# Kernel tuning notes

Measured on AMD Instinct MI355X. Metric: run time of the kernel, lower is better.

The kernel has to match this reference:

```python
import jax, jax.numpy as jnp
import numpy as np

B, L, D_MODEL = 4, 2048, 1024
N_HEADS, FEAT, HEAD_DIM = 16, 16, 64
CHUNK = 128
EPS = 1e-12


def taylor_exp(x):
    """2nd-order Taylor feature map of exp(q.k/sqrt(d)).
    x: (b, h, l, f) -> (b, h, l, 1 + f + f*f)"""
    f = x.shape[-1]
    r2 = jnp.sqrt(jnp.asarray(2.0, x.dtype))
    rd = jnp.sqrt(jnp.asarray(float(f), x.dtype))      # sqrt(d)
    rrd = jnp.sqrt(rd)                                  # d**0.25
    x2 = (x[..., :, None] * x[..., None, :]).reshape(*x.shape[:-1], f * f) / r2
    ones = jnp.ones_like(x[..., :1])
    return jnp.concatenate([ones, x / rrd, x2 / rd], axis=-1)


def setup_inputs() -> dict:
    key = jax.random.key(0)
    k1, k2, k3, k4, k5 = jax.random.split(key, 5)
    s = 0.02
    return {
        "hidden_states": jax.random.normal(k1, (B, L, D_MODEL), jnp.float32),
        "Wq": jax.random.normal(k2, (N_HEADS * FEAT, D_MODEL), jnp.float32) * s,
        "Wk": jax.random.normal(k3, (N_HEADS * FEAT, D_MODEL), jnp.float32) * s,
        "Wv": jax.random.normal(k4, (N_HEADS * HEAD_DIM, D_MODEL), jnp.float32) * s,
        "Wo": jax.random.normal(k5, (D_MODEL, N_HEADS * HEAD_DIM), jnp.float32) * s,
    }


def reference(hidden_states, Wq, Wk, Wv, Wo):
    b, l, _ = hidden_states.shape
    # projections (Linear without bias: x @ W.T)
    q = (hidden_states @ Wq.T).reshape(b, l, N_HEADS, FEAT).transpose(0, 2, 1, 3)
    k = (hidden_states @ Wk.T).reshape(b, l, N_HEADS, FEAT).transpose(0, 2, 1, 3)
    v = (hidden_states @ Wv.T).reshape(b, l, N_HEADS, HEAD_DIM).transpose(0, 2, 1, 3)

    qf = taylor_exp(q)  # (b, h, l, De) with De = 1 + f + f^2 = 273
    kf = taylor_exp(k)
    De = qf.shape[-1]

    # chunked causal linear attention: same math as cumulative kv-state
    n = l // CHUNK
    qc = jnp.moveaxis(qf.reshape(b, N_HEADS, n, CHUNK, De), 2, 0)       # (n,b,h,c,De)
    kc = jnp.moveaxis(kf.reshape(b, N_HEADS, n, CHUNK, De), 2, 0)
    vc = jnp.moveaxis(v.reshape(b, N_HEADS, n, CHUNK, HEAD_DIM), 2, 0)
    mask = jnp.tril(jnp.ones((CHUNK, CHUNK), qf.dtype))

    def step(carry, xs):
        S, z = carry                       # S: (b,h,De,e), z: (b,h,De)
        qi, ki, vi = xs
        attn = jnp.einsum('bhid,bhjd->bhij', qi, ki) * mask
        num = jnp.einsum('bhij,bhje->bhie', attn, vi) \
            + jnp.einsum('bhid,bhde->bhie', qi, S)
        den = attn.sum(-1) + jnp.einsum('bhid,bhd->bhi', qi, z)
        yi = num / (den[..., None] + EPS)
        S = S + jnp.einsum('bhjd,bhje->bhde', ki, vi)
        z = z + ki.sum(2)
        return (S, z), yi

    S0 = jnp.zeros((b, N_HEADS, De, HEAD_DIM), qf.dtype)
    z0 = jnp.zeros((b, N_HEADS, De), qf.dtype)
    _, ys = jax.lax.scan(step, (S0, z0), (qc, kc, vc))
    y = jnp.moveaxis(ys, 0, 2).reshape(b, N_HEADS, l, HEAD_DIM)          # (b,h,l,e)
    y = y.transpose(0, 2, 1, 3).reshape(b, l, N_HEADS * HEAD_DIM)        # (b,l,h*e)
    return y @ Wo.T
```

## Files before the change

### kernel.cpp

```cpp
#include <hip/hip_runtime.h>
#include <hip/hip_bf16.h>

#define BB 4
#define LL 2048
#define DM 1024
#define NH 16
#define FEAT 16
#define HD 64
#define CHUNK 128
#define NCHUNK 16
#define NEXT 65
#define SROW 18720
#define EPS 1e-12f
#define INV_R2RD 0.17677669529663688f
#define QKVLD 1536

typedef short bf16x8_t __attribute__((ext_vector_type(8)));
typedef float f32x4_t  __attribute__((ext_vector_type(4)));

__device__ __forceinline__ float b2f(unsigned short u) {
    union { unsigned int i; float f; } x; x.i = ((unsigned int)u) << 16; return x.f;
}
__device__ __forceinline__ unsigned short f2b(float f) {
    __hip_bfloat16 h = __float2bfloat16(f);
    return *reinterpret_cast<unsigned short*>(&h);
}

__global__ __launch_bounds__(256)
void cast_all(const float* __restrict__ hs, const float* __restrict__ wq,
              const float* __restrict__ wk, const float* __restrict__ wv,
              const float* __restrict__ wo, unsigned short* __restrict__ hs_bf,
              unsigned short* __restrict__ wqkv, unsigned short* __restrict__ wo_bf)
{
    const int i = (blockIdx.x * 256 + threadIdx.x) * 4;
    const float* s; unsigned short* d;
    if (i < 8388608)       { s = hs + i;             d = hs_bf + i; }
    else if (i < 8650752)  { s = wq + (i - 8388608); d = wqkv + (i - 8388608); }
    else if (i < 8912896)  { s = wk + (i - 8650752); d = wqkv + 262144 + (i - 8650752); }
    else if (i < 9961472)  { s = wv + (i - 8912896); d = wqkv + 524288 + (i - 8912896); }
    else if (i < 11010048) { s = wo + (i - 9961472); d = wo_bf + (i - 9961472); }
    else return;
    float4 v = *(const float4*)s;
    ushort4 o; o.x = f2b(v.x); o.y = f2b(v.y); o.z = f2b(v.z); o.w = f2b(v.w);
    *(ushort4*)d = o;
}

template <typename OutT>
__global__ __launch_bounds__(512, 2)
void gemm_bf16_8ph(const unsigned short* __restrict__ A, const unsigned short* __restrict__ Bw,
                   OutT* __restrict__ C, int K, int lda, int ldb, int ldc)
{
    __shared__ unsigned short lds[65536];
    const int tid  = threadIdx.x;
    const int wid  = tid >> 6, lane = tid & 63;
    const int wm   = wid >> 2, wn = wid & 3;
    const int ml   = lane & 15, quad = lane >> 4;
    const int nwg = gridDim.x * gridDim.y;
    const int lin = blockIdx.y * gridDim.x + blockIdx.x;
    const int swz_id = (lin & 7) * (nwg >> 3) + (lin >> 3);
    const int m0   = (swz_id / gridDim.x) * 256, n0 = (swz_id % gridDim.x) * 256;
    const int NT   = K >> 6;

    const int srow  = tid >> 3;
    const int scol  = ((tid & 7) ^ (srow & 7)) << 3;
    const int wbase = wid << 9;

    auto stage_half = [&](int t, int isB, int h) {
        const unsigned short* g0 = isB ? Bw : A;
        const int ld = isB ? ldb : lda;
        const int rb = (isB ? n0 : m0) + h * 128 + srow;
        const int k0 = t << 6;
        unsigned short* lb = lds + (isB ? 32768 : 0) + ((t & 1) << 14) + (h << 13) + wbase;
#pragma unroll
        for (int l = 0; l < 2; ++l) {
            const unsigned short* g = g0 + (size_t)(rb + l * 64) * ld + k0 + scol;
            __builtin_amdgcn_global_load_lds((const __attribute__((address_space(1))) void*)g,
                                             (__attribute__((address_space(3))) void*)(lb + l * 4096),
                                             16, 0, 0);
        }
    };

    f32x4_t acc[8][4];
#pragma unroll
    for (int i = 0; i < 8; ++i)
#pragma unroll
        for (int j = 0; j < 4; ++j) acc[i][j] = (f32x4_t){0.f, 0.f, 0.f, 0.f};

    stage_half(0, 0, 0); stage_half(0, 1, 0); stage_half(0, 0, 1); stage_half(0, 1, 1);
    stage_half(1, 0, 0); stage_half(1, 1, 0); stage_half(1, 0, 1);
    asm volatile("s_waitcnt vmcnt(6)" ::: "memory");
    __builtin_amdgcn_s_barrier();

    const int swz  = (ml & 7) << 3;
    const int c0   = (quad << 3) ^ swz;
    const int c1   = (32 + (quad << 3)) ^ swz;
    const int arow = ml << 6;

    bf16x8_t aA[4][2], bLo[2][2], bHi[2][2];

    for (int t = 0; t < NT; ++t) {
        const int ab = (t & 1) << 14;
        const int bb = 32768 + ((t & 1) << 14);

#pragma unroll
        for (int m = 0; m < 4; ++m) {
            const int r = ab + ((2 * m + wm) << 10) + arow;
            aA[m][0] = *(const bf16x8_t*)&lds[r + c0];
            aA[m][1] = *(const bf16x8_t*)&lds[r + c1];
        }
#pragma unroll
        for (int n = 0; n < 2; ++n) {
            const int r = bb + ((4 * n + wn) << 10) + arow;
            bLo[n][0] = *(const bf16x8_t*)&lds[r + c0];
            bLo[n][1] = *(const bf16x8_t*)&lds[r + c1];
        }
        if (t + 1 < NT) stage_half(t + 1, 1, 1);
        __builtin_amdgcn_s_barrier();
        asm volatile("s_waitcnt lgkmcnt(0)" ::: "memory");
        __builtin_amdgcn_sched_barrier(0);
        __builtin_amdgcn_s_setprio(1);
#pragma unroll
        for (int m = 0; m < 4; ++m)
#pragma unroll
            for (int n = 0; n < 2; ++n) {
                acc[m][n] = __builtin_amdgcn_mfma_f32_16x16x32_bf16(aA[m][0], bLo[n][0], acc[m][n], 0, 0, 0);
                acc[m][n] = __builtin_amdgcn_mfma_f32_16x16x32_bf16(aA[m][1], bLo[n][1], acc[m][n], 0, 0, 0);
            }
        __builtin_amdgcn_s_setprio(0);
        __builtin_amdgcn_s_barrier();

#pragma unroll
        for (int n = 0; n < 2; ++n) {
            const int r = bb + ((4 * (n + 2) + wn) << 10) + arow;
            bHi[n][0] = *(const bf16x8_t*)&lds[r + c0];
            bHi[n][1] = *(const bf16x8_t*)&lds[r + c1];
        }
        if (t + 2 < NT) stage_half(t + 2, 0, 0);
        __builtin_amdgcn_s_barrier();
        asm volatile("s_waitcnt lgkmcnt(0)" ::: "memory");
        __builtin_amdgcn_sched_barrier(0);
        __builtin_amdgcn_s_setprio(1);
#pragma unroll
        for (int m = 0; m < 4; ++m)
#pragma unroll
            for (int n = 0; n < 2; ++n) {
                acc[m][2 + n] = __builtin_amdgcn_mfma_f32_16x16x32_bf16(aA[m][0], bHi[n][0], acc[m][2 + n], 0, 0, 0);
                acc[m][2 + n] = __builtin_amdgcn_mfma_f32_16x16x32_bf16(aA[m][1], bHi[n][1], acc[m][2 + n], 0, 0, 0);
            }
        __builtin_amdgcn_s_setprio(0);
        __builtin_amdgcn_s_barrier();

#pragma unroll
        for (int m = 0; m < 4; ++m) {
            const int r = ab + ((2 * (m + 4) + wm) << 10) + arow;
            aA[m][0] = *(const bf16x8_t*)&lds[r + c0];
            aA[m][1] = *(const bf16x8_t*)&lds[r + c1];
        }
        if (t + 2 < NT) stage_half(t + 2, 1, 0);
        __builtin_amdgcn_s_barrier();
        asm volatile("s_waitcnt lgkmcnt(0)" ::: "memory");
        __builtin_amdgcn_sched_barrier(0);
        __builtin_amdgcn_s_setprio(1);
#pragma unroll
        for (int m = 0; m < 4; ++m)
#pragma unroll
            for (int n = 0; n < 2; ++n) {
                acc[4 + m][2 + n] = __builtin_amdgcn_mfma_f32_16x16x32_bf16(aA[m][0], bHi[n][0], acc[4 + m][2 + n], 0, 0, 0);
                acc[4 + m][2 + n] = __builtin_amdgcn_mfma_f32_16x16x32_bf16(aA[m][1], bHi[n][1], acc[4 + m][2 + n], 0, 0, 0);
            }
        __builtin_amdgcn_s_setprio(0);
        __builtin_amdgcn_s_barrier();

        if (t + 2 < NT) stage_half(t + 2, 0, 1);
        __builtin_amdgcn_s_barrier();
        asm volatile("s_waitcnt lgkmcnt(0)" ::: "memory");
        __builtin_amdgcn_sched_barrier(0);
        __builtin_amdgcn_s_setprio(1);
#pragma unroll
        for (int m = 0; m < 4; ++m)
#pragma unroll
            for (int n = 0; n < 2; ++n) {
                acc[4 + m][n] = __builtin_amdgcn_mfma_f32_16x16x32_bf16(aA[m][0], bLo[n][0], acc[4 + m][n], 0, 0, 0);
                acc[4 + m][n] = __builtin_amdgcn_mfma_f32_16x16x32_bf16(aA[m][1], bLo[n][1], acc[4 + m][n], 0, 0, 0);
            }
        __builtin_amdgcn_s_setprio(0);
        if (t + 2 < NT)      asm volatile("s_waitcnt vmcnt(6)" ::: "memory");
        else if (t + 1 < NT) asm volatile("s_waitcnt vmcnt(0)" ::: "memory");
        __builtin_amdgcn_s_barrier();
    }

#pragma unroll
    for (int m = 0; m < 8; ++m) {
        const int rbase = m0 + (2 * m + wm) * 16 + quad * 4;
#pragma unroll
        for (int n = 0; n < 4; ++n) {
            const int col = n0 + (4 * n + wn) * 16 + ml;
#pragma unroll
            for (int r = 0; r < 4; ++r) {
                const float v = acc[m][n][r];
                if constexpr (sizeof(OutT) == 2) {
                    ((unsigned short*)C)[(size_t)(rbase + r) * ldc + col] = f2b(v);
                } else {
                    ((float*)C)[(size_t)(rbase + r) * ldc + col] = v;
                }
            }
        }
    }
}

__global__ __launch_bounds__(512, 2)
void gemm_bf16_128x256(const unsigned short* __restrict__ A, const unsigned short* __restrict__ Bw,
                       float* __restrict__ C, int K, int lda, int ldb, int ldc)
{
    __shared__ unsigned short lds[49152];
    const int tid  = threadIdx.x;
    const int wid  = tid >> 6, lane = tid & 63;
    const int wm   = wid >> 2, wn = wid & 3;
    const int ml   = lane & 15, quad = lane >> 4;
    const int nwg = gridDim.x * gridDim.y;
    const int lin = blockIdx.y * gridDim.x + blockIdx.x;
    const int swz_id = (lin & 7) * (nwg >> 3) + (lin >> 3);
    const int m0   = (swz_id / gridDim.x) * 128, n0 = (swz_id % gridDim.x) * 256;
    const int NT   = K >> 6;

    const int srow  = tid >> 3;
    const int scol  = ((tid & 7) ^ (srow & 7)) << 3;
    const int wbase = wid << 9;

    auto stage_unit = [&](int t, int isB, int u) {
        const unsigned short* g0 = isB ? Bw : A;
        const int ld = isB ? ldb : lda;
        const int rb = (isB ? n0 : m0) + u * 64 + srow;
        const int k0 = t << 6;
        unsigned short* lb = lds + (isB ? 16384 : 0) + ((t & 1) << (isB ? 14 : 13))
                             + (u << 12) + wbase;
        const unsigned short* g = g0 + (size_t)rb * ld + k0 + scol;
        __builtin_amdgcn_global_load_lds((const __attribute__((address_space(1))) void*)g,
                                         (__attribute__((address_space(3))) void*)lb, 16, 0, 0);
    };

    f32x4_t acc[4][4];
#pragma unroll
    for (int i = 0; i < 4; ++i)
#pragma unroll
        for (int j = 0; j < 4; ++j) acc[i][j] = (f32x4_t){0.f, 0.f, 0.f, 0.f};

    stage_unit(0, 0, 0); stage_unit(0, 0, 1);
    stage_unit(0, 1, 0); stage_unit(0, 1, 1); stage_unit(0, 1, 2); stage_unit(0, 1, 3);
    stage_unit(1, 0, 0); stage_unit(1, 0, 1);
    stage_unit(1, 1, 0); stage_unit(1, 1, 1);
    asm volatile("s_waitcnt vmcnt(4)" ::: "memory");
    __builtin_amdgcn_s_barrier();

    const int swz  = (ml & 7) << 3;
    const int c0   = (quad << 3) ^ swz;
    const int c1   = (32 + (quad << 3)) ^ swz;
    const int arow = ml << 6;

    bf16x8_t aA[4][2], bF[2][2];

    for (int t = 0; t < NT; ++t) {
        const int ab = (t & 1) << 13;
        const int bb = 16384 + ((t & 1) << 14);

#pragma unroll
        for (int m = 0; m < 4; ++m) {
            const int r = ab + ((2 * m + wm) << 10) + arow;
            aA[m][0] = *(const bf16x8_t*)&lds[r + c0];
            aA[m][1] = *(const bf16x8_t*)&lds[r + c1];
        }
#pragma unroll
        for (int n = 0; n < 2; ++n) {
            const int r = bb + ((4 * n + wn) << 10) + arow;
            bF[n][0] = *(const bf16x8_t*)&lds[r + c0];
            bF[n][1] = *(const bf16x8_t*)&lds[r + c1];
        }
        if (t + 1 < NT) { stage_unit(t + 1, 1, 2); stage_unit(t + 1, 1, 3); }
        __builtin_amdgcn_s_barrier();
        asm volatile("s_waitcnt lgkmcnt(0)" ::: "memory");
        __builtin_amdgcn_sched_barrier(0);
        __builtin_amdgcn_s_setprio(1);
#pragma unroll
        for (int m = 0; m < 4; ++m)
#pragma unroll
            for (int n = 0; n < 2; ++n) {
                acc[m][n] = __builtin_amdgcn_mfma_f32_16x16x32_bf16(aA[m][0], bF[n][0], acc[m][n], 0, 0, 0);
                acc[m][n] = __builtin_amdgcn_mfma_f32_16x16x32_bf16(aA[m][1], bF[n][1], acc[m][n], 0, 0, 0);
            }
        __builtin_amdgcn_s_setprio(0);
        __builtin_amdgcn_s_barrier();

#pragma unroll
        for (int n = 0; n < 2; ++n) {
            const int r = bb + ((4 * (n + 2) + wn) << 10) + arow;
            bF[n][0] = *(const bf16x8_t*)&lds[r + c0];
            bF[n][1] = *(const bf16x8_t*)&lds[r + c1];
        }
        if (t + 2 < NT) {
            stage_unit(t + 2, 0, 0); stage_unit(t + 2, 0, 1);
            stage_unit(t + 2, 1, 0); stage_unit(t + 2, 1, 1);
        }
        __builtin_amdgcn_s_barrier();
        asm volatile("s_waitcnt lgkmcnt(0)" ::: "memory");
        __builtin_amdgcn_sched_barrier(0);
        __builtin_amdgcn_s_setprio(1);
#pragma unroll
        for (int m = 0; m < 4; ++m)
#pragma unroll
            for (int n = 0; n < 2; ++n) {
                acc[m][2 + n] = __builtin_amdgcn_mfma_f32_16x16x32_bf16(aA[m][0], bF[n][0], acc[m][2 + n], 0, 0, 0);
                acc[m][2 + n] = __builtin_amdgcn_mfma_f32_16x16x32_bf16(aA[m][1], bF[n][1], acc[m][2 + n], 0, 0, 0);
            }
        __builtin_amdgcn_s_setprio(0);
        if (t + 2 < NT)      asm volatile("s_waitcnt vmcnt(4)" ::: "memory");
        else if (t + 1 < NT) asm volatile("s_waitcnt vmcnt(0)" ::: "memory");
        __builtin_amdgcn_s_barrier();
    }

#pragma unroll
    for (int m = 0; m < 4; ++m) {
        const int rbase = m0 + (2 * m + wm) * 16 + quad * 4;
#pragma unroll
        for (int n = 0; n < 4; ++n) {
            const int col = n0 + (4 * n + wn) * 16 + ml;
#pragma unroll
            for (int r = 0; r < 4; ++r)
                C[(size_t)(rbase + r) * ldc + col] = acc[m][n][r];
        }
    }
}

__global__ __launch_bounds__(256)
void state_kernel(const unsigned short* __restrict__ qkv, unsigned short* __restrict__ STg)
{
    __shared__ unsigned short KT[16 * 136];
    __shared__ unsigned short VT[80 * 136];

    const int x = blockIdx.x;
    const int c = x & 15, bh = x >> 4;
    const int b = bh >> 4, h = bh & 15;
    const int tid = threadIdx.x;
    const int wave = tid >> 6, lane = tid & 63;
    const int ml = lane & 15, kg8 = (lane >> 4) * 8;
    const int quad4 = (lane >> 4) * 4;
    const size_t rowbase = (size_t)(b * LL + c * CHUNK);
    const size_t Sbase = (size_t)x * SROW;

    {
        const int row = tid >> 1, half = tid & 1;
        uint4 kv = *(const uint4*)(qkv + (rowbase + row) * QKVLD + 256 + h * 16 + half * 8);
        const unsigned short* kp = (const unsigned short*)&kv;
#pragma unroll
        for (int i = 0; i < 8; ++i) KT[(half * 8 + i) * 136 + row] = kp[i];
#pragma unroll
        for (int cc = 0; cc < 4; ++cc) {
            uint4 vv = *(const uint4*)(qkv + (rowbase + row) * QKVLD + 512 + h * 64 + half * 32 + cc * 8);
            const unsigned short* vp = (const unsigned short*)&vv;
#pragma unroll
            for (int i = 0; i < 8; ++i) VT[(half * 32 + cc * 8 + i) * 136 + row] = vp[i];
        }
        if (half == 0) {
            VT[64 * 136 + row] = 0x3F80;
        } else {
#pragma unroll
            for (int e = 65; e < 80; ++e) VT[e * 136 + row] = 0;
        }
    }
    __syncthreads();

    bf16x8_t bfr[5][4];
#pragma unroll
    for (int nt = 0; nt < 5; ++nt)
#pragma unroll
        for (int ks = 0; ks < 4; ++ks)
            bfr[nt][ks] = *(const bf16x8_t*)&VT[(nt * 16 + ml) * 136 + ks * 32 + kg8];

    for (int mt = wave; mt < 18; mt += 4) {
        const int d = mt * 16 + ml;
        bf16x8_t af[4];
#pragma unroll
        for (int ks = 0; ks < 4; ++ks) {
            const int jb = ks * 32 + kg8;
            unsigned short o[8];
            if (d >= 24 && d < 280) {
                const int e = d - 24, a = e >> 4, bq = e & 15;
                bf16x8_t ka = *(const bf16x8_t*)&KT[a  * 136 + jb];
                bf16x8_t kb = *(const bf16x8_t*)&KT[bq * 136 + jb];
#pragma unroll
                for (int j = 0; j < 8; ++j)
                    o[j] = f2b(b2f((unsigned short)ka[j]) * b2f((unsigned short)kb[j]) * INV_R2RD);
            } else if (d == 0) {
#pragma unroll
                for (int j = 0; j < 8; ++j) o[j] = 0x3F80;
            } else if (d <= 16) {
                bf16x8_t kx = *(const bf16x8_t*)&KT[(d - 1) * 136 + jb];
#pragma unroll
                for (int j = 0; j < 8; ++j) o[j] = f2b(b2f((unsigned short)kx[j]) * 0.5f);
            } else {
#pragma unroll
                for (int j = 0; j < 8; ++j) o[j] = 0;
            }
            af[ks] = *(const bf16x8_t*)o;
        }
        f32x4_t acc[5];
#pragma unroll
        for (int nt = 0; nt < 5; ++nt) acc[nt] = (f32x4_t){0.f, 0.f, 0.f, 0.f};
        __builtin_amdgcn_s_setprio(1);
#pragma unroll
        for (int nt = 0; nt < 5; ++nt)
#pragma unroll
            for (int ks = 0; ks < 4; ++ks)
                acc[nt] = __builtin_amdgcn_mfma_f32_16x16x32_bf16(af[ks], bfr[nt][ks], acc[nt], 0, 0, 0);
        __builtin_amdgcn_s_setprio(0);
#pragma unroll
        for (int nt = 0; nt < 5; ++nt) {
            ushort4 pk;
            pk.x = f2b(acc[nt][0]); pk.y = f2b(acc[nt][1]);
            pk.z = f2b(acc[nt][2]); pk.w = f2b(acc[nt][3]);
            if (nt < 4) {
                *(ushort4*)(STg + Sbase + (size_t)mt * 1040 + (nt * 16 + ml) * 16 + quad4) = pk;
            } else if (ml == 0) {
                *(ushort4*)(STg + Sbase + (size_t)mt * 1040 + 1024 + quad4) = pk;
            }
        }
    }
}

__global__ __launch_bounds__(256)
void scan_S(unsigned short* __restrict__ STg) {
    const int bh  = blockIdx.y;
    const int idx = blockIdx.x * 256 + threadIdx.x;
    if (idx >= SROW / 8) return;
    const size_t base = (size_t)bh * NCHUNK * SROW + (size_t)idx * 8;
    uint4 v[NCHUNK];
#pragma unroll
    for (int c = 0; c < NCHUNK; ++c)
        v[c] = *(const uint4*)(STg + base + (size_t)c * SROW);
    float acc[8] = {};
#pragma unroll
    for (int c = 0; c < NCHUNK; ++c) {
        const unsigned short* vp = (const unsigned short*)&v[c];
        uint4 o;
        unsigned short* op = (unsigned short*)&o;
#pragma unroll
        for (int i = 0; i < 8; ++i) { op[i] = f2b(acc[i]); acc[i] += b2f(vp[i]); }
        *(uint4*)(STg + base + (size_t)c * SROW) = o;
    }
}

#define OFF_VT 0
#define OFF_QP 0
#define OFF_KP 5120
#define OFF_A  10880

__global__ __launch_bounds__(256)
void out_kernel(const unsigned short* __restrict__ qkv_ro, const unsigned short* __restrict__ STg,
                unsigned short* __restrict__ qkv_w)
{
    __shared__ unsigned short smem[28288];

    const int x = blockIdx.x;
    const int c = x & 15, bh = x >> 4;
    const int b = bh >> 4, h = bh & 15;
    const int tid = threadIdx.x;
    const int w = tid >> 6, lane = tid & 63;
    const int ml = lane & 15, quad = lane >> 4, kg8 = quad * 8;
    const size_t rowbase = (size_t)(b * LL + c * CHUNK);
    const size_t Sbase = (size_t)x * SROW;

    const unsigned short* stp = STg + Sbase + (size_t)(quad >> 1) * 1040 + (quad & 1) * 8;
    bf16x8_t stf[3][5];
    auto ldst = [&](int kq, int slot) {
#pragma unroll
        for (int nt = 0; nt < 5; ++nt)
            stf[slot][nt] = *(const bf16x8_t*)(stp + (size_t)kq * 2080 + (nt * 16 + ml) * 16);
    };

    const int row = tid >> 1, half = tid & 1;
    uint4 qv = *(const uint4*)(qkv_ro + (rowbase + row) * QKVLD + h * 16 + half * 8);
    uint4 kv = *(const uint4*)(qkv_ro + (rowbase + row) * QKVLD + 256 + h * 16 + half * 8);
    uint4 vreg[4];
#pragma unroll
    for (int cc = 0; cc < 4; ++cc)
        vreg[cc] = *(const uint4*)(qkv_ro + (rowbase + row) * QKVLD + 512 + h * 64 + half * 32 + cc * 8);
    ldst(0, 0);
    ldst(1, 1);

    *(uint4*)&smem[OFF_QP + row * 40 + half * 8] = qv;
    *(uint4*)&smem[OFF_QP + row * 40 + 16 + half * 8] = (uint4){0, 0, 0, 0};
    *(uint4*)&smem[OFF_KP + row * 40 + half * 8] = kv;
    *(uint4*)&smem[OFF_KP + row * 40 + 16 + half * 8] = (uint4){0, 0, 0, 0};
    __syncthreads();

    {
        bf16x8_t q0 = *(const bf16x8_t*)&smem[OFF_QP + (w * 32 + ml) * 40 + kg8];
        bf16x8_t q1 = *(const bf16x8_t*)&smem[OFF_QP + (w * 32 + 16 + ml) * 40 + kg8];
#pragma unroll
        for (int nt = 0; nt < 8; ++nt) {
            bf16x8_t kf = *(const bf16x8_t*)&smem[OFF_KP + (nt * 16 + ml) * 40 + kg8];
            f32x4_t a0 = __builtin_amdgcn_mfma_f32_16x16x32_bf16(q0, kf, (f32x4_t){0,0,0,0}, 0, 0, 0);
            f32x4_t a1 = __builtin_amdgcn_mfma_f32_16x16x32_bf16(q1, kf, (f32x4_t){0,0,0,0}, 0, 0, 0);
            const int j = nt * 16 + ml;
#pragma unroll
            for (int r = 0; r < 4; ++r) {
                int i0 = w * 32 + quad * 4 + r;
                float s0 = a0[r] * 0.25f;
                float v0 = (j <= i0) ? (1.f + s0 + 0.5f * s0 * s0) : 0.f;
                smem[OFF_A + i0 * 136 + j] = f2b(v0);
                int i1 = i0 + 16;
                float s1 = a1[r] * 0.25f;
                float v1 = (j <= i1) ? (1.f + s1 + 0.5f * s1 * s1) : 0.f;
                smem[OFF_A + i1 * 136 + j] = f2b(v1);
            }
        }
    }
    const int r0 = w * 32 + ml, r1 = r0 + 16;
    float qA[16], qB[16];
    {
        bf16x8_t t0 = *(const bf16x8_t*)&smem[OFF_QP + r0 * 40];
        bf16x8_t t1 = *(const bf16x8_t*)&smem[OFF_QP + r0 * 40 + 8];
        bf16x8_t t2 = *(const bf16x8_t*)&smem[OFF_QP + r1 * 40];
        bf16x8_t t3 = *(const bf16x8_t*)&smem[OFF_QP + r1 * 40 + 8];
#pragma unroll
        for (int i = 0; i < 8; ++i) {
            qA[i] = b2f((unsigned short)t0[i]); qA[8 + i] = b2f((unsigned short)t1[i]);
            qB[i] = b2f((unsigned short)t2[i]); qB[8 + i] = b2f((unsigned short)t3[i]);
        }
    }
    float qselA[8], qselB[8];
#pragma unroll
    for (int j = 0; j < 8; ++j) {
        qselA[j] = (quad & 1) ? qA[j] : qA[8 + j];
        qselB[j] = (quad & 1) ? qB[j] : qB[8 + j];
    }
    __syncthreads();

    {
#pragma unroll
        for (int cc = 0; cc < 4; ++cc) {
            const unsigned short* vp = (const unsigned short*)&vreg[cc];
#pragma unroll
            for (int i = 0; i < 8; ++i) smem[OFF_VT + (half * 32 + cc * 8 + i) * 136 + row] = vp[i];
        }
        if (half == 0) {
            smem[OFF_VT + 64 * 136 + row] = 0x3F80;
        } else {
#pragma unroll
            for (int e = 65; e < 80; ++e) smem[OFF_VT + e * 136 + row] = 0;
        }
    }
    __syncthreads();

    f32x4_t acc[2][5];
#pragma unroll
    for (int mt = 0; mt < 2; ++mt)
#pragma unroll
        for (int nt = 0; nt < 5; ++nt) acc[mt][nt] = (f32x4_t){0.f, 0.f, 0.f, 0.f};

    ldst(2, 2);

#pragma unroll
    for (int ks = 0; ks < 4; ++ks) {
        bf16x8_t af0 = *(const bf16x8_t*)&smem[OFF_A + (w * 32 + ml) * 136 + ks * 32 + kg8];
        bf16x8_t af1 = *(const bf16x8_t*)&smem[OFF_A + (w * 32 + 16 + ml) * 136 + ks * 32 + kg8];
        __builtin_amdgcn_s_setprio(1);
#pragma unroll
        for (int nt = 0; nt < 5; ++nt) {
            bf16x8_t bv = *(const bf16x8_t*)&smem[OFF_VT + (nt * 16 + ml) * 136 + ks * 32 + kg8];
            acc[0][nt] = __builtin_amdgcn_mfma_f32_16x16x32_bf16(af0, bv, acc[0][nt], 0, 0, 0);
            acc[1][nt] = __builtin_amdgcn_mfma_f32_16x16x32_bf16(af1, bv, acc[1][nt], 0, 0, 0);
        }
        __builtin_amdgcn_s_setprio(0);
    }

#pragma unroll
    for (int kq = 0; kq < 9; ++kq) {
        bf16x8_t qf[2];
#pragma unroll
        for (int mt = 0; mt < 2; ++mt) {
            const float* q    = (mt == 0) ? qA : qB;
            const float* qsel = (mt == 0) ? qselA : qselB;
            const int d0 = kq * 32 + kg8;
            unsigned short o[8];
            if (d0 >= 24 && d0 < 280) {
                const int i2 = 2 * kq;
                const float base = (quad == 3) ? q[i2 > 15 ? 15 : i2]
                                 : (quad == 0) ? q[i2 < 2 ? 0 : i2 - 2]
                                               : q[i2 < 1 ? 0 : i2 - 1];
                const float qa = base * INV_R2RD;
#pragma unroll
                for (int j = 0; j < 8; ++j) o[j] = f2b(qa * qsel[j]);
            } else if (d0 == 0) {
                o[0] = 0x3F80;
#pragma unroll
                for (int j = 1; j < 8; ++j) o[j] = f2b(q[j - 1] * 0.5f);
            } else if (d0 == 8) {
#pragma unroll
                for (int j = 0; j < 8; ++j) o[j] = f2b(q[7 + j] * 0.5f);
            } else if (d0 == 16) {
                o[0] = f2b(q[15] * 0.5f);
#pragma unroll
                for (int j = 1; j < 8; ++j) o[j] = 0;
            } else {
#pragma unroll
                for (int j = 0; j < 8; ++j) o[j] = 0;
            }
            qf[mt] = *(const bf16x8_t*)o;
        }
        __builtin_amdgcn_s_setprio(1);
#pragma unroll
        for (int nt = 0; nt < 5; ++nt) {
            acc[0][nt] = __builtin_amdgcn_mfma_f32_16x16x32_bf16(qf[0], stf[kq % 3][nt], acc[0][nt], 0, 0, 0);
            acc[1][nt] = __builtin_amdgcn_mfma_f32_16x16x32_bf16(qf[1], stf[kq % 3][nt], acc[1][nt], 0, 0, 0);
        }
        __builtin_amdgcn_s_setprio(0);
        if (kq + 3 < 9) ldst(kq + 3, kq % 3);
    }

#pragma unroll
    for (int mt = 0; mt < 2; ++mt) {
        float den[4];
#pragma unroll
        for (int r = 0; r < 4; ++r) den[r] = __shfl(acc[mt][4][r], lane & 48);
#pragma unroll
        for (int r = 0; r < 4; ++r) {
            const size_t grow = rowbase + w * 32 + mt * 16 + quad * 4 + r;
            const float rc = 1.f / (den[r] + EPS);
#pragma unroll
            for (int nt = 0; nt < 4; ++nt)
                qkv_w[grow * QKVLD + 512 + h * 64 + nt * 16 + ml] = f2b(acc[mt][nt][r] * rc);
        }
    }
}

extern "C" void kernel_launch(void* const* d_in, const int* in_sizes, int n_in,
                              void* d_out, int out_size, void* d_ws, size_t ws_size,
                              hipStream_t stream)
{
    (void)in_sizes; (void)n_in; (void)out_size; (void)ws_size;
    const float* hs = (const float*)d_in[0];
    const float* Wq = (const float*)d_in[1];
    const float* Wk = (const float*)d_in[2];
    const float* Wv = (const float*)d_in[3];
    const float* Wo = (const float*)d_in[4];
    float* out = (float*)d_out;

    char* ws = (char*)d_ws;
    unsigned short* STg   = (unsigned short*)ws;
    unsigned short* hs_bf = (unsigned short*)ws;
    size_t off = 47185920;
    unsigned short* qkv   = (unsigned short*)(ws + off); off += 25165824;
    unsigned short* Wqkv  = (unsigned short*)(ws + off); off += 3145728;
    unsigned short* Wo_bf = (unsigned short*)(ws + off); off += 2097152;

    cast_all<<<10752, 256, 0, stream>>>(hs, Wq, Wk, Wv, Wo, hs_bf, Wqkv, Wo_bf);
    gemm_bf16_8ph<unsigned short><<<dim3(6, 32), 512, 0, stream>>>(hs_bf, Wqkv, qkv,
                                                                   DM, DM, DM, QKVLD);
    state_kernel<<<1024, 256, 0, stream>>>(qkv, STg);
    scan_S<<<dim3(10, 64), 256, 0, stream>>>(STg);
    out_kernel<<<1024, 256, 0, stream>>>(qkv, STg, qkv);
    gemm_bf16_128x256<<<dim3(4, 64), 512, 0, stream>>>(qkv + 512, Wo_bf, out,
                                                       DM, QKVLD, DM, DM);
}
```

Baseline: 198.3 us.

## Fuse chunk state computation with prefix scan and retile QKV GEMM to 256x192

The per-chunk KV-state kernel and the separate scan kernel become one kernel. Each block walks the 16 chunks of a (batch, head) in order, keeps the running state in MFMA accumulators, writes the exclusive prefix, and prefetches the next chunk's K/V from global memory. This removes a launch and a full read/write pass over the state buffer, but it cuts the grid from 1024 blocks to 256 and serialises the chunk loop. Separately, the QKV projection GEMM now uses 256x192 tiles on an 8x32 grid, so 256 blocks are launched instead of 192 to fill more CUs, with the phase schedule reworked to match.

```diff
diff --git a/kernel.cpp b/kernel.cpp
--- a/kernel.cpp
+++ b/kernel.cpp
@@ -45,12 +45,11 @@
     *(ushort4*)d = o;
 }
 
-template <typename OutT>
 __global__ __launch_bounds__(512, 2)
-void gemm_bf16_8ph(const unsigned short* __restrict__ A, const unsigned short* __restrict__ Bw,
-                   OutT* __restrict__ C, int K, int lda, int ldb, int ldc)
+void gemm_bf16_192(const unsigned short* __restrict__ A, const unsigned short* __restrict__ Bw,
+                   unsigned short* __restrict__ C, int K, int lda, int ldb, int ldc)
 {
-    __shared__ unsigned short lds[65536];
+    __shared__ unsigned short lds[57344];
     const int tid  = threadIdx.x;
     const int wid  = tid >> 6, lane = tid & 63;
     const int wm   = wid >> 2, wn = wid & 3;
@@ -58,36 +57,35 @@
     const int nwg = gridDim.x * gridDim.y;
     const int lin = blockIdx.y * gridDim.x + blockIdx.x;
     const int swz_id = (lin & 7) * (nwg >> 3) + (lin >> 3);
-    const int m0   = (swz_id / gridDim.x) * 256, n0 = (swz_id % gridDim.x) * 256;
+    const int m0   = (swz_id / gridDim.x) * 256, n0 = (swz_id % gridDim.x) * 192;
     const int NT   = K >> 6;
 
     const int srow  = tid >> 3;
     const int scol  = ((tid & 7) ^ (srow & 7)) << 3;
     const int wbase = wid << 9;
 
-    auto stage_half = [&](int t, int isB, int h) {
+    auto stage_unit = [&](int t, int isB, int u) {
         const unsigned short* g0 = isB ? Bw : A;
         const int ld = isB ? ldb : lda;
-        const int rb = (isB ? n0 : m0) + h * 128 + srow;
-        const int k0 = t << 6;
-        unsigned short* lb = lds + (isB ? 32768 : 0) + ((t & 1) << 14) + (h << 13) + wbase;
-#pragma unroll
-        for (int l = 0; l < 2; ++l) {
-            const unsigned short* g = g0 + (size_t)(rb + l * 64) * ld + k0 + scol;
-            __builtin_amdgcn_global_load_lds((const __attribute__((address_space(1))) void*)g,
-                                             (__attribute__((address_space(3))) void*)(lb + l * 4096),
-                                             16, 0, 0);
-        }
+        const int rb = (isB ? n0 : m0) + u * 64 + srow;
+        unsigned short* lb = lds + (isB ? 32768 + (t & 1) * 12288 : ((t & 1) << 14))
+                             + (u << 12) + wbase;
+        const unsigned short* g = g0 + (size_t)rb * ld + (t << 6) + scol;
+        __builtin_amdgcn_global_load_lds((const __attribute__((address_space(1))) void*)g,
+                                         (__attribute__((address_space(3))) void*)lb, 16, 0, 0);
     };
 
-    f32x4_t acc[8][4];
+    f32x4_t acc[8][3];
 #pragma unroll
     for (int i = 0; i < 8; ++i)
 #pragma unroll
-        for (int j = 0; j < 4; ++j) acc[i][j] = (f32x4_t){0.f, 0.f, 0.f, 0.f};
-
-    stage_half(0, 0, 0); stage_half(0, 1, 0); stage_half(0, 0, 1); stage_half(0, 1, 1);
-    stage_half(1, 0, 0); stage_half(1, 1, 0); stage_half(1, 0, 1);
+        for (int j = 0; j < 3; ++j) acc[i][j] = (f32x4_t){0.f, 0.f, 0.f, 0.f};
+
+    stage_unit(0, 0, 0); stage_unit(0, 0, 1); stage_unit(0, 0, 2); stage_unit(0, 0, 3);
+    stage_unit(0, 1, 0); stage_unit(0, 1, 1); stage_unit(0, 1, 2);
+    stage_unit(1, 0, 0); stage_unit(1, 0, 1);
+    stage_unit(1, 1, 0); stage_unit(1, 1, 1);
+    stage_unit(1, 0, 2); stage_unit(1, 0, 3);
     asm volatile("s_waitcnt vmcnt(6)" ::: "memory");
     __builtin_amdgcn_s_barrier();
 
@@ -96,11 +94,11 @@
     const int c1   = (32 + (quad << 3)) ^ swz;
     const int arow = ml << 6;
 
-    bf16x8_t aA[4][2], bLo[2][2], bHi[2][2];
+    bf16x8_t aA[4][2], bLo[2][2], bN2[2];
 
     for (int t = 0; t < NT; ++t) {
         const int ab = (t & 1) << 14;
-        const int bb = 32768 + ((t & 1) << 14);
+        const int bb = 32768 + (t & 1) * 12288;
 
 #pragma unroll
         for (int m = 0; m < 4; ++m) {
@@ -110,11 +108,11 @@
         }
 #pragma unroll
         for (int n = 0; n < 2; ++n) {
-            const int r = bb + ((4 * n + wn) << 10) + arow;
+            const int r = bb + (wn * 48 + n * 16 + ml) * 64;
             bLo[n][0] = *(const bf16x8_t*)&lds[r + c0];
             bLo[n][1] = *(const bf16x8_t*)&lds[r + c1];
         }
-        if (t + 1 < NT) stage_half(t + 1, 1, 1);
+        if (t + 1 < NT) stage_unit(t + 1, 1, 2);
         __builtin_amdgcn_s_barrier();
         asm volatile("s_waitcnt lgkmcnt(0)" ::: "memory");
         __builtin_amdgcn_sched_barrier(0);
@@ -129,24 +127,21 @@
         __builtin_amdgcn_s_setprio(0);
         __builtin_amdgcn_s_barrier();
 
-#pragma unroll
-        for (int n = 0; n < 2; ++n) {
-            const int r = bb + ((4 * (n + 2) + wn) << 10) + arow;
-            bHi[n][0] = *(const bf16x8_t*)&lds[r + c0];
-            bHi[n][1] = *(const bf16x8_t*)&lds[r + c1];
-        }
-        if (t + 2 < NT) stage_half(t + 2, 0, 0);
+        {
+            const int r = bb + (wn * 48 + 32 + ml) * 64;
+            bN2[0] = *(const bf16x8_t*)&lds[r + c0];
+            bN2[1] = *(const bf16x8_t*)&lds[r + c1];
+        }
+        if (t + 2 < NT) { stage_unit(t + 2, 0, 0); stage_unit(t + 2, 0, 1); }
         __builtin_amdgcn_s_barrier();
         asm volatile("s_waitcnt lgkmcnt(0)" ::: "memory");
         __builtin_amdgcn_sched_barrier(0);
         __builtin_amdgcn_s_setprio(1);
 #pragma unroll
-        for (int m = 0; m < 4; ++m)
-#pragma unroll
-            for (int n = 0; n < 2; ++n) {
-                acc[m][2 + n] = __builtin_amdgcn_mfma_f32_16x16x32_bf16(aA[m][0], bHi[n][0], acc[m][2 + n], 0, 0, 0);
-                acc[m][2 + n] = __builtin_amdgcn_mfma_f32_16x16x32_bf16(aA[m][1], bHi[n][1], acc[m][2 + n], 0, 0, 0);
-            }
+        for (int m = 0; m < 4; ++m) {
+            acc[m][2] = __builtin_amdgcn_mfma_f32_16x16x32_bf16(aA[m][0], bN2[0], acc[m][2], 0, 0, 0);
+            acc[m][2] = __builtin_amdgcn_mfma_f32_16x16x32_bf16(aA[m][1], bN2[1], acc[m][2], 0, 0, 0);
+        }
         __builtin_amdgcn_s_setprio(0);
         __builtin_amdgcn_s_barrier();
 
@@ -156,22 +151,7 @@
             aA[m][0] = *(const bf16x8_t*)&lds[r + c0];
             aA[m][1] = *(const bf16x8_t*)&lds[r + c1];
         }
-        if (t + 2 < NT) stage_half(t + 2, 1, 0);
-        __builtin_amdgcn_s_barrier();
-        asm volatile("s_waitcnt lgkmcnt(0)" ::: "memory");
-        __builtin_amdgcn_sched_barrier(0);
-        __builtin_amdgcn_s_setprio(1);
-#pragma unroll
-        for (int m = 0; m < 4; ++m)
-#pragma unroll
-            for (int n = 0; n < 2; ++n) {
-                acc[4 + m][2 + n] = __builtin_amdgcn_mfma_f32_16x16x32_bf16(aA[m][0], bHi[n][0], acc[4 + m][2 + n], 0, 0, 0);
-                acc[4 + m][2 + n] = __builtin_amdgcn_mfma_f32_16x16x32_bf16(aA[m][1], bHi[n][1], acc[4 + m][2 + n], 0, 0, 0);
-            }
-        __builtin_amdgcn_s_setprio(0);
-        __builtin_amdgcn_s_barrier();
-
-        if (t + 2 < NT) stage_half(t + 2, 0, 1);
+        if (t + 2 < NT) { stage_unit(t + 2, 1, 0); stage_unit(t + 2, 1, 1); }
         __builtin_amdgcn_s_barrier();
         asm volatile("s_waitcnt lgkmcnt(0)" ::: "memory");
         __builtin_amdgcn_sched_barrier(0);
@@ -184,6 +164,19 @@
                 acc[4 + m][n] = __builtin_amdgcn_mfma_f32_16x16x32_bf16(aA[m][1], bLo[n][1], acc[4 + m][n], 0, 0, 0);
             }
         __builtin_amdgcn_s_setprio(0);
+        __builtin_amdgcn_s_barrier();
+
+        if (t + 2 < NT) { stage_unit(t + 2, 0, 2); stage_unit(t + 2, 0, 3); }
+        __builtin_amdgcn_s_barrier();
+        asm volatile("s_waitcnt lgkmcnt(0)" ::: "memory");
+        __builtin_amdgcn_sched_barrier(0);
+        __builtin_amdgcn_s_setprio(1);
+#pragma unroll
+        for (int m = 0; m < 4; ++m) {
+            acc[4 + m][2] = __builtin_amdgcn_mfma_f32_16x16x32_bf16(aA[m][0], bN2[0], acc[4 + m][2], 0, 0, 0);
+            acc[4 + m][2] = __builtin_amdgcn_mfma_f32_16x16x32_bf16(aA[m][1], bN2[1], acc[4 + m][2], 0, 0, 0);
+        }
+        __builtin_amdgcn_s_setprio(0);
         if (t + 2 < NT)      asm volatile("s_waitcnt vmcnt(6)" ::: "memory");
         else if (t + 1 < NT) asm volatile("s_waitcnt vmcnt(0)" ::: "memory");
         __builtin_amdgcn_s_barrier();
@@ -193,17 +186,11 @@
     for (int m = 0; m < 8; ++m) {
         const int rbase = m0 + (2 * m + wm) * 16 + quad * 4;
 #pragma unroll
-        for (int n = 0; n < 4; ++n) {
-            const int col = n0 + (4 * n + wn) * 16 + ml;
-#pragma unroll
-            for (int r = 0; r < 4; ++r) {
-                const float v = acc[m][n][r];
-                if constexpr (sizeof(OutT) == 2) {
-                    ((unsigned short*)C)[(size_t)(rbase + r) * ldc + col] = f2b(v);
-                } else {
-                    ((float*)C)[(size_t)(rbase + r) * ldc + col] = v;
-                }
-            }
+        for (int n = 0; n < 3; ++n) {
+            const int col = n0 + wn * 48 + n * 16 + ml;
+#pragma unroll
+            for (int r = 0; r < 4; ++r)
+                C[(size_t)(rbase + r) * ldc + col] = f2b(acc[m][n][r]);
         }
     }
 }
@@ -331,51 +318,47 @@
 }
 
 __global__ __launch_bounds__(256)
-void state_kernel(const unsigned short* __restrict__ qkv, unsigned short* __restrict__ STg)
+void state_scan(const unsigned short* __restrict__ qkv, unsigned short* __restrict__ STg)
 {
     __shared__ unsigned short KT[16 * 136];
     __shared__ unsigned short VT[80 * 136];
 
-    const int x = blockIdx.x;
-    const int c = x & 15, bh = x >> 4;
+    const int g  = blockIdx.x & 3, bh = blockIdx.x >> 2;
     const int b = bh >> 4, h = bh & 15;
     const int tid = threadIdx.x;
     const int wave = tid >> 6, lane = tid & 63;
-    const int ml = lane & 15, kg8 = (lane >> 4) * 8;
-    const int quad4 = (lane >> 4) * 4;
-    const size_t rowbase = (size_t)(b * LL + c * CHUNK);
-    const size_t Sbase = (size_t)x * SROW;
-
+    const int ml = lane & 15, kg8 = (lane >> 4) * 8, quad4 = (lane >> 4) * 4;
+    const int mtA = g + 4 * wave;
+    const bool hasB = (wave == 0) && (g < 2);
+    const int mtB = 16 + g;
+
+    const int row = tid >> 1, half = tid & 1;
+    const unsigned short* src = qkv + (size_t)(b * LL) * QKVLD;
+
+    if (half == 0) {
+        VT[64 * 136 + row] = 0x3F80;
+    } else {
+#pragma unroll
+        for (int e = 65; e < 80; ++e) VT[e * 136 + row] = 0;
+    }
+
+    uint4 kvn, vvn[4];
     {
-        const int row = tid >> 1, half = tid & 1;
-        uint4 kv = *(const uint4*)(qkv + (rowbase + row) * QKVLD + 256 + h * 16 + half * 8);
-        const unsigned short* kp = (const unsigned short*)&kv;
-#pragma unroll
-        for (int i = 0; i < 8; ++i) KT[(half * 8 + i) * 136 + row] = kp[i];
-#pragma unroll
-        for (int cc = 0; cc < 4; ++cc) {
-            uint4 vv = *(const uint4*)(qkv + (rowbase + row) * QKVLD + 512 + h * 64 + half * 32 + cc * 8);
-            const unsigned short* vp = (const unsigned short*)&vv;
-#pragma unroll
-            for (int i = 0; i < 8; ++i) VT[(half * 32 + cc * 8 + i) * 136 + row] = vp[i];
-        }
-        if (half == 0) {
-            VT[64 * 136 + row] = 0x3F80;
-        } else {
-#pragma unroll
-            for (int e = 65; e < 80; ++e) VT[e * 136 + row] = 0;
-        }
-    }
-    __syncthreads();
-
-    bf16x8_t bfr[5][4];
-#pragma unroll
-    for (int nt = 0; nt < 5; ++nt)
-#pragma unroll
-        for (int ks = 0; ks < 4; ++ks)
-            bfr[nt][ks] = *(const bf16x8_t*)&VT[(nt * 16 + ml) * 136 + ks * 32 + kg8];
-
-    for (int mt = wave; mt < 18; mt += 4) {
+        const size_t rg = (size_t)row * QKVLD;
+        kvn = *(const uint4*)(src + rg + 256 + h * 16 + half * 8);
+#pragma unroll
+        for (int cc = 0; cc < 4; ++cc)
+            vvn[cc] = *(const uint4*)(src + rg + 512 + h * 64 + half * 32 + cc * 8);
+    }
+
+    f32x4_t prefA[5], prefB[5];
+#pragma unroll
+    for (int nt = 0; nt < 5; ++nt) {
+        prefA[nt] = (f32x4_t){0.f, 0.f, 0.f, 0.f};
+        prefB[nt] = (f32x4_t){0.f, 0.f, 0.f, 0.f};
+    }
+
+    auto do_tile = [&](int mt, f32x4_t* pref, size_t Sb) {
         const int d = mt * 16 + ml;
         bf16x8_t af[4];
 #pragma unroll
@@ -402,49 +385,57 @@
             }
             af[ks] = *(const bf16x8_t*)o;
         }
-        f32x4_t acc[5];
-#pragma unroll
-        for (int nt = 0; nt < 5; ++nt) acc[nt] = (f32x4_t){0.f, 0.f, 0.f, 0.f};
-        __builtin_amdgcn_s_setprio(1);
+        bf16x8_t bfr[5][4];
 #pragma unroll
         for (int nt = 0; nt < 5; ++nt)
 #pragma unroll
             for (int ks = 0; ks < 4; ++ks)
-                acc[nt] = __builtin_amdgcn_mfma_f32_16x16x32_bf16(af[ks], bfr[nt][ks], acc[nt], 0, 0, 0);
-        __builtin_amdgcn_s_setprio(0);
+                bfr[nt][ks] = *(const bf16x8_t*)&VT[(nt * 16 + ml) * 136 + ks * 32 + kg8];
 #pragma unroll
         for (int nt = 0; nt < 5; ++nt) {
             ushort4 pk;
-            pk.x = f2b(acc[nt][0]); pk.y = f2b(acc[nt][1]);
-            pk.z = f2b(acc[nt][2]); pk.w = f2b(acc[nt][3]);
+            pk.x = f2b(pref[nt][0]); pk.y = f2b(pref[nt][1]);
+            pk.z = f2b(pref[nt][2]); pk.w = f2b(pref[nt][3]);
             if (nt < 4) {
-                *(ushort4*)(STg + Sbase + (size_t)mt * 1040 + (nt * 16 + ml) * 16 + quad4) = pk;
+                *(ushort4*)(STg + Sb + (size_t)mt * 1040 + (nt * 16 + ml) * 16 + quad4) = pk;
             } else if (ml == 0) {
-                *(ushort4*)(STg + Sbase + (size_t)mt * 1040 + 1024 + quad4) = pk;
-            }
-        }
-    }
-}
-
-__global__ __launch_bounds__(256)
-void scan_S(unsigned short* __restrict__ STg) {
-    const int bh  = blockIdx.y;
-    const int idx = blockIdx.x * 256 + threadIdx.x;
-    if (idx >= SROW / 8) return;
-    const size_t base = (size_t)bh * NCHUNK * SROW + (size_t)idx * 8;
-    uint4 v[NCHUNK];
-#pragma unroll
-    for (int c = 0; c < NCHUNK; ++c)
-        v[c] = *(const uint4*)(STg + base + (size_t)c * SROW);
-    float acc[8] = {};
-#pragma unroll
+                *(ushort4*)(STg + Sb + (size_t)mt * 1040 + 1024 + quad4) = pk;
+            }
+        }
+        __builtin_amdgcn_s_setprio(1);
+#pragma unroll
+        for (int nt = 0; nt < 5; ++nt)
+#pragma unroll
+            for (int ks = 0; ks < 4; ++ks)
+                pref[nt] = __builtin_amdgcn_mfma_f32_16x16x32_bf16(af[ks], bfr[nt][ks], pref[nt], 0, 0, 0);
+        __builtin_amdgcn_s_setprio(0);
+    };
+
     for (int c = 0; c < NCHUNK; ++c) {
-        const unsigned short* vp = (const unsigned short*)&v[c];
-        uint4 o;
-        unsigned short* op = (unsigned short*)&o;
-#pragma unroll
-        for (int i = 0; i < 8; ++i) { op[i] = f2b(acc[i]); acc[i] += b2f(vp[i]); }
-        *(uint4*)(STg + base + (size_t)c * SROW) = o;
+        {
+            const unsigned short* kp = (const unsigned short*)&kvn;
+#pragma unroll
+            for (int i = 0; i < 8; ++i) KT[(half * 8 + i) * 136 + row] = kp[i];
+#pragma unroll
+            for (int cc = 0; cc < 4; ++cc) {
+                const unsigned short* vp = (const unsigned short*)&vvn[cc];
+#pragma unroll
+                for (int i = 0; i < 8; ++i) VT[(half * 32 + cc * 8 + i) * 136 + row] = vp[i];
+            }
+        }
+        __syncthreads();
+        if (c + 1 < NCHUNK) {
+            const size_t rg = (size_t)((c + 1) * CHUNK + row) * QKVLD;
+            kvn = *(const uint4*)(src + rg + 256 + h * 16 + half * 8);
+#pragma unroll
+            for (int cc = 0; cc < 4; ++cc)
+                vvn[cc] = *(const uint4*)(src + rg + 512 + h * 64 + half * 32 + cc * 8);
+        }
+
+        const size_t Sb = (size_t)(bh * NCHUNK + c) * SROW;
+        do_tile(mtA, prefA, Sb);
+        if (hasB) do_tile(mtB, prefB, Sb);
+        __syncthreads();
     }
 }
 
@@ -654,10 +645,9 @@
     unsigned short* Wo_bf = (unsigned short*)(ws + off); off += 2097152;
 
     cast_all<<<10752, 256, 0, stream>>>(hs, Wq, Wk, Wv, Wo, hs_bf, Wqkv, Wo_bf);
-    gemm_bf16_8ph<unsigned short><<<dim3(6, 32), 512, 0, stream>>>(hs_bf, Wqkv, qkv,
-                                                                   DM, DM, DM, QKVLD);
-    state_kernel<<<1024, 256, 0, stream>>>(qkv, STg);
-    scan_S<<<dim3(10, 64), 256, 0, stream>>>(STg);
+    gemm_bf16_192<<<dim3(8, 32), 512, 0, stream>>>(hs_bf, Wqkv, qkv,
+                                                   DM, DM, DM, QKVLD);
+    state_scan<<<256, 256, 0, stream>>>(qkv, STg);
     out_kernel<<<1024, 256, 0, stream>>>(qkv, STg, qkv);
     gemm_bf16_128x256<<<dim3(4, 64), 512, 0, stream>>>(qkv + 512, Wo_bf, out,
                                                        DM, QKVLD, DM, DM);
```

After: 202.8 us. 2.3% more time.
